# Kernel tuning notes

Hardware: AMD Instinct MI355X
Metric: run time of the kernel (lower is better)

The kernel has to match this reference:

```python
import jax, jax.numpy as jnp
import numpy as np

# Loss hyperparameters (from init_kwargs defaults)
ALPHA, BETA, GAMMA = 1.0, 2.0, 1.0
DAY_W, NIGHT_W = 2.0, 0.5
PEAK_WIN_W, PEAK_WIN = 3.0, 2
HIGH_POWER_W, POWER_PCT = 1.5, 0.75
HOURS = 24

B, S = 4096, 4032  # seq_len = 24 * 168 days


def setup_inputs() -> dict:
    key = jax.random.key(0)
    k1, k2 = jax.random.split(key)
    y_true = jax.random.uniform(k1, (B, S), dtype=jnp.float32)
    # predictions = truth + noise, clipped to be realistic power values
    y_pred = y_true + 0.1 * jax.random.normal(k2, (B, S), dtype=jnp.float32)
    return {"y_pred": y_pred, "y_true": y_true}


def _daily_peaks(y, day_mask):
    # y, day_mask: (B, D, H). Peaks restricted to daytime hours.
    masked = jnp.where(day_mask, y, jnp.float32(-1e9))
    times = jnp.argmax(masked, axis=-1)                                   # (B, D) int
    vals = jnp.take_along_axis(y, times[..., None], axis=-1)[..., 0]      # (B, D)
    return times, vals


def reference(y_pred, y_true):
    b, s = y_true.shape
    d = s // HOURS
    # default is_daytime: hour-of-day in [6, 20]
    hour = jnp.arange(HOURS, dtype=jnp.int32)
    day_hour_mask = (hour >= 6) & (hour <= 20)                            # (H,)
    is_daytime = jnp.broadcast_to(day_hour_mask[None, None, :], (b, d, HOURS))

    yt = y_true.reshape(b, d, HOURS)
    yp = y_pred.reshape(b, d, HOURS)

    true_times, true_peaks = _daily_peaks(yt, is_daytime)
    pred_times, pred_peaks = _daily_peaks(yp, is_daytime)
    peak_time_errors = (pred_times - true_times).astype(jnp.float32)      # (B, D)

    # --- step weights: day/night base, x PEAK_WIN_W in [peak-2, peak+2] ---
    base_w = jnp.where(is_daytime, jnp.float32(DAY_W), jnp.float32(NIGHT_W))  # (B,D,H)
    pt = true_times[..., None]                                            # (B,D,1)
    in_window = (hour[None, None, :] >= pt - PEAK_WIN) & (hour[None, None, :] <= pt + PEAK_WIN)
    step_w = base_w * jnp.where(in_window, jnp.float32(PEAK_WIN_W), jnp.float32(1.0))
    step_w = step_w.reshape(b, s)

    sq_err = (y_pred - y_true) ** 2
    L_overall = jnp.sum(sq_err * step_w) / jnp.sum(step_w)

    # --- peak magnitude loss with high-power sample weighting ---
    sample_avg_peaks = jnp.mean(true_peaks, axis=1)                       # (B,)
    thr = jnp.quantile(sample_avg_peaks, POWER_PCT)
    high = sample_avg_peaks > thr                                         # (B,) bool
    sample_w = jnp.where(high[:, None], jnp.float32(HIGH_POWER_W), jnp.float32(1.0))
    sample_w = jnp.broadcast_to(sample_w, true_peaks.shape)               # (B, D)
    peak_sq = (pred_peaks - true_peaks) ** 2
    L_peak_mag = jnp.sum(peak_sq * sample_w) / jnp.sum(sample_w)

    L_peak_timing = jnp.mean(jnp.abs(peak_time_errors) * 10.0)

    return ALPHA * L_overall + BETA * L_peak_mag + GAMMA * L_peak_timing
```

## Files before the change

kernel.cpp:

```cpp
#include <hip/hip_runtime.h>
#include <math.h>

#define HOURS   24
#define DPS     168
#define S_LEN   4032
#define DPC     10
#define NBLK    2048
#define NWAVES  (NBLK * 4)
#define NB_MAX  4096


__global__ __launch_bounds__(256, 8) void day_kernel(
    const float* __restrict__ yTrue, const float* __restrict__ yPred,
    float* __restrict__ Aday, float* __restrict__ Pday,
    float* __restrict__ SEp, float* __restrict__ SWp, float* __restrict__ Tp,
    long long totalDays, int nChunks)
{
    const int lane = threadIdx.x & 63;
    const int wIdx = (blockIdx.x << 2) | (threadIdx.x >> 6);
    const int base = (lane / 6) * 6;
    const int j    = lane - base;
    const bool laneActive = (lane < 60);

    float se = 0.f, sw = 0.f, te = 0.f;

    float4 nT = make_float4(0.f, 0.f, 0.f, 0.f);
    float4 nP = make_float4(0.f, 0.f, 0.f, 0.f);
    int c = wIdx;
    if (c < nChunks) {
        long long d = (long long)c * DPC + (base / 6);
        bool v = laneActive && (d < totalDays);
        size_t off = v ? ((size_t)d * HOURS + 4 * j) : 0;
        nT = *(const float4*)(yTrue + off);
        nP = *(const float4*)(yPred + off);
    }

    for (; c < nChunks; c += NWAVES) {
        float4 cT = nT, cP = nP;
        int cn = c + NWAVES;
        if (cn < nChunks) {
            long long d2 = (long long)cn * DPC + (base / 6);
            bool v2 = laneActive && (d2 < totalDays);
            size_t off2 = v2 ? ((size_t)d2 * HOURS + 4 * j) : 0;
            nT = *(const float4*)(yTrue + off2);
            nP = *(const float4*)(yPred + off2);
        }

        const long long d = (long long)c * DPC + (base / 6);
        const bool valid = laneActive && (d < totalDays);

        float yt[4] = {cT.x, cT.y, cT.z, cT.w};
        float yp[4] = {cP.x, cP.y, cP.z, cP.w};

        float tv = -1e30f, pv = -1e30f; int th = 0, ph = 0;
#pragma unroll
        for (int k = 0; k < 4; ++k) {
            int h = 4 * j + k;
            bool dayh = (h >= 6) && (h <= 20);
            if (dayh && yt[k] > tv) { tv = yt[k]; th = h; }
            if (dayh && yp[k] > pv) { pv = yp[k]; ph = h; }
        }
        if (!valid) { tv = -1e30f; pv = -1e30f; }

        float m1t = fmaxf(tv, __shfl_xor(tv, 1, 64));
        float m1p = fmaxf(pv, __shfl_xor(pv, 1, 64));
        float gmt = fmaxf(fmaxf(__shfl(m1t, base, 64), __shfl(m1t, base + 2, 64)),
                          __shfl(m1t, base + 4, 64));
        float gmp = fmaxf(fmaxf(__shfl(m1p, base, 64), __shfl(m1p, base + 2, 64)),
                          __shfl(m1p, base + 4, 64));

        unsigned long long blt = __ballot(valid && (tv == gmt));
        unsigned long long blp = __ballot(valid && (pv == gmp));
        int ft = __ffsll(blt >> base) - 1;
        int fp = __ffsll(blp >> base) - 1;
        int tt = __shfl(th, base + ft, 64);
        int pt = __shfl(ph, base + fp, 64);

        if (valid) {
#pragma unroll
            for (int k = 0; k < 4; ++k) {
                int h = 4 * j + k;
                float bw = ((h >= 6) && (h <= 20)) ? 2.0f : 0.5f;
                float wgt = bw * (((h >= tt - 2) && (h <= tt + 2)) ? 3.0f : 1.0f);
                float dd = yp[k] - yt[k];
                se = fmaf(wgt * dd, dd, se);
                sw += wgt;
            }
            if (j == 0) {
                te += fabsf((float)(pt - tt));
                Aday[d] = gmt;
                float dpk = gmp - gmt;
                Pday[d] = dpk * dpk;
            }
        }
    }

#pragma unroll
    for (int o = 32; o > 0; o >>= 1) {
        se += __shfl_down(se, o, 64);
        sw += __shfl_down(sw, o, 64);
        te += __shfl_down(te, o, 64);
    }
    if (lane == 0) { SEp[wIdx] = se; SWp[wIdx] = sw; Tp[wIdx] = te; }
}


__global__ __launch_bounds__(64) void sample_kernel(
    const float* __restrict__ Aday, const float* __restrict__ Pday,
    float* __restrict__ A, float* __restrict__ P)
{
    const int b = blockIdx.x;
    const int lane = threadIdx.x;
    const float* ad = Aday + (size_t)b * DPS;
    const float* pd = Pday + (size_t)b * DPS;
    float sa = 0.f, sp = 0.f;
    for (int i = lane; i < DPS; i += 64) { sa += ad[i]; sp += pd[i]; }
#pragma unroll
    for (int o = 32; o > 0; o >>= 1) {
        sa += __shfl_down(sa, o, 64);
        sp += __shfl_down(sp, o, 64);
    }
    if (lane == 0) { A[b] = sa * (1.0f / (float)DPS); P[b] = sp; }
}


__global__ __launch_bounds__(256) void rank_kernel(
    const float* __restrict__ A, float* __restrict__ qout, int nB)
{
    __shared__ float sA[NB_MAX];
    const int tid = threadIdx.x;

    for (int i = tid; i < nB; i += 256) sA[i] = A[i];
    __syncthreads();

    const int b = blockIdx.x * 128 + (tid >> 1);
    const int half = tid & 1;
    if (b >= nB) return;
    const float v = sA[b];
    const int span = nB / 2;
    const float4* s4 = (const float4*)(sA + half * span);

    int cl = 0, ce = 0;
    for (int i = 0; i < span / 4; ++i) {
        float4 x = s4[i];
        cl += (x.x < v) + (x.y < v) + (x.z < v) + (x.w < v);
        ce += (x.x == v) + (x.y == v) + (x.z == v) + (x.w == v);
    }
    cl += __shfl_xor(cl, 1, 64);
    ce += __shfl_xor(ce, 1, 64);

    if (half == 0) {
        double pos = 0.75 * (double)(nB - 1);
        int lo = (int)pos;
        int hi = (lo + 1 < nB) ? lo + 1 : lo;
        if (lo >= cl && lo < cl + ce) qout[0] = v;
        if (hi >= cl && hi < cl + ce) qout[1] = v;
    }
}


__device__ inline double block_reduce_d(double v, double* scratch, int tid) {
#pragma unroll
    for (int o = 32; o > 0; o >>= 1) v += __shfl_down(v, o, 64);
    if ((tid & 63) == 0) scratch[tid >> 6] = v;
    __syncthreads();
    double r = 0.0;
    if (tid == 0) r = scratch[0] + scratch[1] + scratch[2] + scratch[3];
    __syncthreads();
    return r;
}

__global__ __launch_bounds__(256) void final_kernel(
    const float* __restrict__ SEp, const float* __restrict__ SWp,
    const float* __restrict__ Tp, const float* __restrict__ P,
    const float* __restrict__ A, const float* __restrict__ qout,
    float* __restrict__ out, int nB, int nW)
{
    __shared__ double s_dred[4];
    const int tid = threadIdx.x;

    double pos = 0.75 * (double)(nB - 1);
    double frac = pos - (double)((int)pos);
    float thr = (float)((double)qout[0] + frac * ((double)qout[1] - (double)qout[0]));

    double se = 0.0, sw = 0.0, te = 0.0, wp = 0.0, wsum = 0.0;
    for (int i = tid; i < nW; i += 256) {
        se += (double)SEp[i];
        sw += (double)SWp[i];
        te += (double)Tp[i];
    }
    for (int b = tid; b < nB; b += 256) {
        float w = (A[b] > thr) ? 1.5f : 1.0f;
        wp   += (double)w * (double)P[b];
        wsum += (double)w;
    }
    se   = block_reduce_d(se,   s_dred, tid);
    sw   = block_reduce_d(sw,   s_dred, tid);
    te   = block_reduce_d(te,   s_dred, tid);
    wp   = block_reduce_d(wp,   s_dred, tid);
    wsum = block_reduce_d(wsum, s_dred, tid);

    if (tid == 0) {
        double L_overall = se / sw;
        double L_peak    = wp / ((double)DPS * wsum);
        double L_timing  = 10.0 * te / ((double)nB * (double)DPS);
        out[0] = (float)(L_overall + 2.0 * L_peak + L_timing);
    }
}


extern "C" void kernel_launch(void* const* d_in, const int* in_sizes, int n_in,
                              void* d_out, int out_size, void* d_ws, size_t ws_size,
                              hipStream_t stream) {
    const float* y_pred = (const float*)d_in[0];
    const float* y_true = (const float*)d_in[1];
    int total = in_sizes[0];
    int nB = total / S_LEN;
    long long totalDays = (long long)nB * DPS;
    int nChunks = (int)((totalDays + DPC - 1) / DPC);

    float* ws   = (float*)d_ws;
    float* Aday = ws;
    float* Pday = Aday + (size_t)totalDays;
    float* SEp  = Pday + (size_t)totalDays;
    float* SWp  = SEp + NWAVES;
    float* Tp   = SWp + NWAVES;
    float* A    = Tp  + NWAVES;
    float* P    = A   + (size_t)nB;
    float* q    = P   + (size_t)nB;

    day_kernel<<<NBLK, 256, 0, stream>>>(y_true, y_pred, Aday, Pday, SEp, SWp, Tp,
                                         totalDays, nChunks);
    sample_kernel<<<nB, 64, 0, stream>>>(Aday, Pday, A, P);
    rank_kernel<<<(nB + 127) / 128, 256, 0, stream>>>(A, q, nB);
    final_kernel<<<1, 256, 0, stream>>>(SEp, SWp, Tp, P, A, q, (float*)d_out, nB, NWAVES);
}
```

Baseline: 185.9 us.

## Map one day per thread in day kernel and split rank counting four ways

The day kernel now gives each thread a whole 24-hour day: it loads six float4s per input and finds the argmax serially, replacing the earlier scheme of six lanes per day with shuffles and ballots. Per-block partial sums are reduced through shared memory, and the grid becomes one block per 256 days instead of a fixed persistent grid. The rank kernel splits each sample's count across four threads instead of two. Per-thread loads are strided by 96 bytes, which may hurt coalescing, and register use rises to hold 48 floats.

After: 169.7 us. 8.7% less time.

```diff
diff --git a/kernel.cpp b/kernel.cpp
--- a/kernel.cpp
+++ b/kernel.cpp
@@ -4,95 +4,67 @@
 #define HOURS   24
 #define DPS     168
 #define S_LEN   4032
-#define DPC     10
-#define NBLK    2048
-#define NWAVES  (NBLK * 4)
 #define NB_MAX  4096
 
 
-__global__ __launch_bounds__(256, 8) void day_kernel(
+__global__ __launch_bounds__(256) void day_kernel(
     const float* __restrict__ yTrue, const float* __restrict__ yPred,
     float* __restrict__ Aday, float* __restrict__ Pday,
-    float* __restrict__ SEp, float* __restrict__ SWp, float* __restrict__ Tp,
-    long long totalDays, int nChunks)
-{
-    const int lane = threadIdx.x & 63;
-    const int wIdx = (blockIdx.x << 2) | (threadIdx.x >> 6);
-    const int base = (lane / 6) * 6;
-    const int j    = lane - base;
-    const bool laneActive = (lane < 60);
-
-    float se = 0.f, sw = 0.f, te = 0.f;
-
-    float4 nT = make_float4(0.f, 0.f, 0.f, 0.f);
-    float4 nP = make_float4(0.f, 0.f, 0.f, 0.f);
-    int c = wIdx;
-    if (c < nChunks) {
-        long long d = (long long)c * DPC + (base / 6);
-        bool v = laneActive && (d < totalDays);
-        size_t off = v ? ((size_t)d * HOURS + 4 * j) : 0;
-        nT = *(const float4*)(yTrue + off);
-        nP = *(const float4*)(yPred + off);
-    }
-
-    for (; c < nChunks; c += NWAVES) {
-        float4 cT = nT, cP = nP;
-        int cn = c + NWAVES;
-        if (cn < nChunks) {
-            long long d2 = (long long)cn * DPC + (base / 6);
-            bool v2 = laneActive && (d2 < totalDays);
-            size_t off2 = v2 ? ((size_t)d2 * HOURS + 4 * j) : 0;
-            nT = *(const float4*)(yTrue + off2);
-            nP = *(const float4*)(yPred + off2);
-        }
-
-        const long long d = (long long)c * DPC + (base / 6);
-        const bool valid = laneActive && (d < totalDays);
-
-        float yt[4] = {cT.x, cT.y, cT.z, cT.w};
-        float yp[4] = {cP.x, cP.y, cP.z, cP.w};
-
-        float tv = -1e30f, pv = -1e30f; int th = 0, ph = 0;
-#pragma unroll
-        for (int k = 0; k < 4; ++k) {
-            int h = 4 * j + k;
-            bool dayh = (h >= 6) && (h <= 20);
-            if (dayh && yt[k] > tv) { tv = yt[k]; th = h; }
-            if (dayh && yp[k] > pv) { pv = yp[k]; ph = h; }
-        }
-        if (!valid) { tv = -1e30f; pv = -1e30f; }
-
-        float m1t = fmaxf(tv, __shfl_xor(tv, 1, 64));
-        float m1p = fmaxf(pv, __shfl_xor(pv, 1, 64));
-        float gmt = fmaxf(fmaxf(__shfl(m1t, base, 64), __shfl(m1t, base + 2, 64)),
-                          __shfl(m1t, base + 4, 64));
-        float gmp = fmaxf(fmaxf(__shfl(m1p, base, 64), __shfl(m1p, base + 2, 64)),
-                          __shfl(m1p, base + 4, 64));
-
-        unsigned long long blt = __ballot(valid && (tv == gmt));
-        unsigned long long blp = __ballot(valid && (pv == gmp));
-        int ft = __ffsll(blt >> base) - 1;
-        int fp = __ffsll(blp >> base) - 1;
-        int tt = __shfl(th, base + ft, 64);
-        int pt = __shfl(ph, base + fp, 64);
-
-        if (valid) {
-#pragma unroll
-            for (int k = 0; k < 4; ++k) {
-                int h = 4 * j + k;
-                float bw = ((h >= 6) && (h <= 20)) ? 2.0f : 0.5f;
-                float wgt = bw * (((h >= tt - 2) && (h <= tt + 2)) ? 3.0f : 1.0f);
-                float dd = yp[k] - yt[k];
-                se = fmaf(wgt * dd, dd, se);
-                sw += wgt;
-            }
-            if (j == 0) {
-                te += fabsf((float)(pt - tt));
-                Aday[d] = gmt;
-                float dpk = gmp - gmt;
-                Pday[d] = dpk * dpk;
-            }
-        }
+    float* __restrict__ SEb, float* __restrict__ SWb, float* __restrict__ Tb,
+    long long totalDays)
+{
+    __shared__ float s_red[3][4];
+    const int tid = threadIdx.x;
+    const int lane = tid & 63;
+    const int wv = tid >> 6;
+
+    const long long d = (long long)blockIdx.x * 256 + tid;
+    const bool valid = d < totalDays;
+    const long long dc = valid ? d : 0;
+
+    const float4* gt = (const float4*)(yTrue + dc * HOURS);
+    const float4* gp = (const float4*)(yPred + dc * HOURS);
+
+    float4 t0 = gt[0], t1 = gt[1], t2 = gt[2], t3 = gt[3], t4 = gt[4], t5 = gt[5];
+    float4 p0 = gp[0], p1 = gp[1], p2 = gp[2], p3 = gp[3], p4 = gp[4], p5 = gp[5];
+
+    float yt[24], yp[24];
+    yt[0]=t0.x; yt[1]=t0.y; yt[2]=t0.z; yt[3]=t0.w;
+    yt[4]=t1.x; yt[5]=t1.y; yt[6]=t1.z; yt[7]=t1.w;
+    yt[8]=t2.x; yt[9]=t2.y; yt[10]=t2.z; yt[11]=t2.w;
+    yt[12]=t3.x; yt[13]=t3.y; yt[14]=t3.z; yt[15]=t3.w;
+    yt[16]=t4.x; yt[17]=t4.y; yt[18]=t4.z; yt[19]=t4.w;
+    yt[20]=t5.x; yt[21]=t5.y; yt[22]=t5.z; yt[23]=t5.w;
+    yp[0]=p0.x; yp[1]=p0.y; yp[2]=p0.z; yp[3]=p0.w;
+    yp[4]=p1.x; yp[5]=p1.y; yp[6]=p1.z; yp[7]=p1.w;
+    yp[8]=p2.x; yp[9]=p2.y; yp[10]=p2.z; yp[11]=p2.w;
+    yp[12]=p3.x; yp[13]=p3.y; yp[14]=p3.z; yp[15]=p3.w;
+    yp[16]=p4.x; yp[17]=p4.y; yp[18]=p4.z; yp[19]=p4.w;
+    yp[20]=p5.x; yp[21]=p5.y; yp[22]=p5.z; yp[23]=p5.w;
+
+    float tbest = yt[6]; int tt = 6;
+#pragma unroll
+    for (int h = 7; h <= 20; ++h) if (yt[h] > tbest) { tbest = yt[h]; tt = h; }
+    float pbest = yp[6]; int pt = 6;
+#pragma unroll
+    for (int h = 7; h <= 20; ++h) if (yp[h] > pbest) { pbest = yp[h]; pt = h; }
+
+    float se = 0.f, sw = 0.f;
+#pragma unroll
+    for (int h = 0; h < 24; ++h) {
+        float bw = ((h >= 6) && (h <= 20)) ? 2.0f : 0.5f;
+        float wgt = bw * (((h >= tt - 2) && (h <= tt + 2)) ? 3.0f : 1.0f);
+        float dd = yp[h] - yt[h];
+        se = fmaf(wgt * dd, dd, se);
+        sw += wgt;
+    }
+    float te = fabsf((float)(pt - tt));
+    if (!valid) { se = 0.f; sw = 0.f; te = 0.f; }
+
+    if (valid) {
+        Aday[d] = tbest;
+        float dpk = pbest - tbest;
+        Pday[d] = dpk * dpk;
     }
 
 #pragma unroll
@@ -101,7 +73,13 @@
         sw += __shfl_down(sw, o, 64);
         te += __shfl_down(te, o, 64);
     }
-    if (lane == 0) { SEp[wIdx] = se; SWp[wIdx] = sw; Tp[wIdx] = te; }
+    if (lane == 0) { s_red[0][wv] = se; s_red[1][wv] = sw; s_red[2][wv] = te; }
+    __syncthreads();
+    if (tid == 0) {
+        SEb[blockIdx.x] = s_red[0][0] + s_red[0][1] + s_red[0][2] + s_red[0][3];
+        SWb[blockIdx.x] = s_red[1][0] + s_red[1][1] + s_red[1][2] + s_red[1][3];
+        Tb[blockIdx.x]  = s_red[2][0] + s_red[2][1] + s_red[2][2] + s_red[2][3];
+    }
 }
 
 
@@ -133,12 +111,12 @@
     for (int i = tid; i < nB; i += 256) sA[i] = A[i];
     __syncthreads();
 
-    const int b = blockIdx.x * 128 + (tid >> 1);
-    const int half = tid & 1;
+    const int b = blockIdx.x * 64 + (tid >> 2);
+    const int quar = tid & 3;
     if (b >= nB) return;
     const float v = sA[b];
-    const int span = nB / 2;
-    const float4* s4 = (const float4*)(sA + half * span);
+    const int span = nB / 4;
+    const float4* s4 = (const float4*)(sA + quar * span);
 
     int cl = 0, ce = 0;
     for (int i = 0; i < span / 4; ++i) {
@@ -146,10 +124,10 @@
         cl += (x.x < v) + (x.y < v) + (x.z < v) + (x.w < v);
         ce += (x.x == v) + (x.y == v) + (x.z == v) + (x.w == v);
     }
-    cl += __shfl_xor(cl, 1, 64);
-    ce += __shfl_xor(ce, 1, 64);
-
-    if (half == 0) {
+    cl += __shfl_xor(cl, 1, 64); ce += __shfl_xor(ce, 1, 64);
+    cl += __shfl_xor(cl, 2, 64); ce += __shfl_xor(ce, 2, 64);
+
+    if (quar == 0) {
         double pos = 0.75 * (double)(nB - 1);
         int lo = (int)pos;
         int hi = (lo + 1 < nB) ? lo + 1 : lo;
@@ -171,10 +149,10 @@
 }
 
 __global__ __launch_bounds__(256) void final_kernel(
-    const float* __restrict__ SEp, const float* __restrict__ SWp,
-    const float* __restrict__ Tp, const float* __restrict__ P,
+    const float* __restrict__ SEb, const float* __restrict__ SWb,
+    const float* __restrict__ Tb, const float* __restrict__ P,
     const float* __restrict__ A, const float* __restrict__ qout,
-    float* __restrict__ out, int nB, int nW)
+    float* __restrict__ out, int nB, int nBlk)
 {
     __shared__ double s_dred[4];
     const int tid = threadIdx.x;
@@ -184,10 +162,10 @@
     float thr = (float)((double)qout[0] + frac * ((double)qout[1] - (double)qout[0]));
 
     double se = 0.0, sw = 0.0, te = 0.0, wp = 0.0, wsum = 0.0;
-    for (int i = tid; i < nW; i += 256) {
-        se += (double)SEp[i];
-        sw += (double)SWp[i];
-        te += (double)Tp[i];
+    for (int i = tid; i < nBlk; i += 256) {
+        se += (double)SEb[i];
+        sw += (double)SWb[i];
+        te += (double)Tb[i];
     }
     for (int b = tid; b < nB; b += 256) {
         float w = (A[b] > thr) ? 1.5f : 1.0f;
@@ -217,21 +195,20 @@
     int total = in_sizes[0];
     int nB = total / S_LEN;
     long long totalDays = (long long)nB * DPS;
-    int nChunks = (int)((totalDays + DPC - 1) / DPC);
+    int nBlk = (int)((totalDays + 255) / 256);
 
     float* ws   = (float*)d_ws;
     float* Aday = ws;
     float* Pday = Aday + (size_t)totalDays;
-    float* SEp  = Pday + (size_t)totalDays;
-    float* SWp  = SEp + NWAVES;
-    float* Tp   = SWp + NWAVES;
-    float* A    = Tp  + NWAVES;
+    float* SEb  = Pday + (size_t)totalDays;
+    float* SWb  = SEb + (size_t)nBlk;
+    float* Tb   = SWb + (size_t)nBlk;
+    float* A    = Tb  + (size_t)nBlk;
     float* P    = A   + (size_t)nB;
     float* q    = P   + (size_t)nB;
 
-    day_kernel<<<NBLK, 256, 0, stream>>>(y_true, y_pred, Aday, Pday, SEp, SWp, Tp,
-                                         totalDays, nChunks);
+    day_kernel<<<nBlk, 256, 0, stream>>>(y_true, y_pred, Aday, Pday, SEb, SWb, Tb, totalDays);
     sample_kernel<<<nB, 64, 0, stream>>>(Aday, Pday, A, P);
-    rank_kernel<<<(nB + 127) / 128, 256, 0, stream>>>(A, q, nB);
-    final_kernel<<<1, 256, 0, stream>>>(SEp, SWp, Tp, P, A, q, (float*)d_out, nB, NWAVES);
-}
+    rank_kernel<<<(nB + 63) / 64, 256, 0, stream>>>(A, q, nB);
+    final_kernel<<<1, 256, 0, stream>>>(SEb, SWb, Tb, P, A, q, (float*)d_out, nB, nBlk);
+}
```
